# Kernel tuning notes

Measured on AMD Instinct MI355X. Metric: run time of the kernel, lower is better.

## Reference

```python
import jax, jax.numpy as jnp
import numpy as np

NMAX = 1
MARGIN = 0.2
N, D = 16384, 256

def setup_inputs() -> dict:
    key = jax.random.key(0)
    k1, k2 = jax.random.split(key)
    imgs = jax.random.normal(k1, (N, D), dtype=jnp.float32)
    caps = jax.random.normal(k2, (N, D), dtype=jnp.float32)
    return {"imgs": imgs, "caps": caps}

def reference(imgs, caps):
    # scores[i, j] = <img_i, cap_j>
    scores = imgs @ caps.T                      # [N, N]
    diag = jnp.diagonal(scores)                 # [N]
    s = scores - 2.0 * jnp.diag(diag)
    # hardest negatives per caption (top over image axis = rows) -> [nmax, N]
    max_c = jax.lax.top_k(s.T, NMAX)[0].T
    # hardest negatives per image (top over caption axis = cols) -> [N, nmax]
    max_i = jax.lax.top_k(s, NMAX)[0]
    neg_cap = jnp.sum(jnp.maximum(max_c + (MARGIN - diag)[None, :], 0.0))
    neg_img = jnp.sum(jnp.maximum(max_i + (MARGIN - diag)[:, None], 0.0))
    return neg_cap + neg_img
```

## Files before the change

### kernel.cpp

```cpp
#include <hip/hip_runtime.h>
#include <hip/hip_bf16.h>
#include <hip/hip_fp8.h>
#include <stdint.h>
#include <math.h>

#define NN 16384
#define DD 256
#define MARGIN_F 0.2f

typedef __attribute__((ext_vector_type(8))) int int32x8;
typedef __attribute__((ext_vector_type(4))) float f32x4;

__device__ inline unsigned fkey(float f) {
    unsigned b = __float_as_uint(f);
    return (b & 0x80000000u) ? ~b : (b | 0x80000000u);
}
__device__ inline float fdec(unsigned k) {
    return __uint_as_float((k & 0x80000000u) ? (k ^ 0x80000000u) : ~k);
}
#define NEG_INF_KEY 0x007FFFFFu

__device__ inline void gload16(const void* g, void* l) {
    __builtin_amdgcn_global_load_lds(
        (const __attribute__((address_space(1))) void*)g,
        (__attribute__((address_space(3))) void*)l, 16, 0, 0);
}

__device__ inline unsigned pk8(float4 v) {
    __hip_fp8_e4m3 q0(v.x), q1(v.y), q2(v.z), q3(v.w);
    return (unsigned)q0.__x | ((unsigned)q1.__x << 8) |
           ((unsigned)q2.__x << 16) | ((unsigned)q3.__x << 24);
}

__global__ __launch_bounds__(256) void fused_prep_kernel(
    const float* __restrict__ imgs, const float* __restrict__ caps,
    unsigned char* __restrict__ imgs8, unsigned char* __restrict__ caps8,
    float* __restrict__ diag, unsigned* __restrict__ rowmax,
    unsigned* __restrict__ colmax) {
    const int i = (blockIdx.x << 2) + (threadIdx.x >> 6);
    const int l = threadIdx.x & 63;
    const float4* a4 = reinterpret_cast<const float4*>(imgs + (size_t)i * DD);
    const float4* b4 = reinterpret_cast<const float4*>(caps + (size_t)i * DD);
    float4 av = a4[l];
    float4 bv = b4[l];
    reinterpret_cast<unsigned*>(imgs8 + (size_t)i * DD)[l] = pk8(av);
    reinterpret_cast<unsigned*>(caps8 + (size_t)i * DD)[l] = pk8(bv);
    float s = av.x * bv.x + av.y * bv.y + av.z * bv.z + av.w * bv.w;
    #pragma unroll
    for (int off = 32; off > 0; off >>= 1) s += __shfl_down(s, off);
    if (l == 0) {
        diag[i] = s;
        rowmax[i] = NEG_INF_KEY;
        colmax[i] = NEG_INF_KEY;
    }
}

__global__ __launch_bounds__(256, 2) void score_max_kernel(
    const unsigned char* __restrict__ imgs8,
    const unsigned char* __restrict__ caps8,
    const float* __restrict__ diag,
    unsigned* __restrict__ rowmax, unsigned* __restrict__ colmax) {

    __shared__ char lds[49152];
    unsigned* clds = reinterpret_cast<unsigned*>(lds + 32768);

    const int bid   = blockIdx.x;
    const int panel = bid >> 2;
    const int strip = bid & 3;
    const int brow  = panel << 7;
    const int scol  = strip << 12;

    const int t    = threadIdx.x;
    const int wid  = t >> 6;
    const int lane = t & 63;
    const int wr   = wid >> 1;
    const int wc   = wid & 1;
    const int rg   = lane >> 4;
    const int cl   = lane & 15;

    #pragma unroll
    for (int i = 0; i < 16; ++i) clds[t + (i << 8)] = NEG_INF_KEY;

    const int sl = t & 15;
    const int rw = t >> 4;
    const int srcoff = (((sl >> 1) ^ (rw & 7)) << 5) + ((sl & 1) << 4);

    {
        const unsigned char* src = imgs8 + (((size_t)(brow + rw)) << 8) + srcoff;
        #pragma unroll
        for (int i = 0; i < 8; ++i)
            gload16(src + ((size_t)i << 12), lds + t * 16 + i * 4096);
    }
    __syncthreads();

    int32x8 af[4][2];
    #pragma unroll
    for (int m = 0; m < 4; ++m) {
        const int row = wr * 64 + m * 16 + cl;
        #pragma unroll
        for (int ks = 0; ks < 2; ++ks)
            af[m][ks] = *reinterpret_cast<const int32x8*>(
                lds + row * 256 + (((rg + (ks << 2)) ^ (cl & 7)) << 5));
    }
    __syncthreads();

    #define STAGEB(bo, cb) {                                                   \
        const unsigned char* s_ =                                              \
            caps8 + (((size_t)((cb) + rw)) << 8) + srcoff;                     \
        _Pragma("unroll")                                                      \
        for (int i_ = 0; i_ < 4; ++i_)                                         \
            gload16(s_ + ((size_t)i_ << 12), lds + (bo) + t * 16 + i_ * 4096); \
    }

    STAGEB(0, scol);

    float rmx[4][4];
    #pragma unroll
    for (int m = 0; m < 4; ++m)
        #pragma unroll
        for (int r = 0; r < 4; ++r) rmx[m][r] = -INFINITY;

    const int rr0 = wc * 32 + cl;
    unsigned boff[2];
    #pragma unroll
    for (int ks = 0; ks < 2; ++ks)
        boff[ks] = rr0 * 256 + (((rg + (ks << 2)) ^ (cl & 7)) << 5);

    const f32x4 zv = (f32x4){0.f, 0.f, 0.f, 0.f};
    #define SCL 0x7F7F7F7F

    for (int h = 0; h < 64; ++h) {
        const int cb = scol + (h << 6);
        const char* cur = lds + ((h & 1) << 14);

        __builtin_amdgcn_s_barrier();
        asm volatile("" ::: "memory");
        if (h < 63) {
            STAGEB(((h + 1) & 1) << 14, cb + 64);
            asm volatile("s_waitcnt vmcnt(4)" ::: "memory");
        } else {
            asm volatile("s_waitcnt vmcnt(0)" ::: "memory");
        }
        __builtin_amdgcn_s_barrier();
        asm volatile("" ::: "memory");

        int32x8 b00 = *reinterpret_cast<const int32x8*>(cur + boff[0]);
        int32x8 b01 = *reinterpret_cast<const int32x8*>(cur + boff[0] + 4096);
        int32x8 b10 = *reinterpret_cast<const int32x8*>(cur + boff[1]);
        int32x8 b11 = *reinterpret_cast<const int32x8*>(cur + boff[1] + 4096);

        f32x4 acc[4][2];
        __builtin_amdgcn_s_setprio(1);
        #pragma unroll
        for (int m = 0; m < 4; ++m) {
            acc[m][0] = __builtin_amdgcn_mfma_scale_f32_16x16x128_f8f6f4(
                af[m][0], b00, zv, 0, 0, 0, SCL, 0, SCL);
            acc[m][1] = __builtin_amdgcn_mfma_scale_f32_16x16x128_f8f6f4(
                af[m][0], b01, zv, 0, 0, 0, SCL, 0, SCL);
        }
        #pragma unroll
        for (int m = 0; m < 4; ++m) {
            acc[m][0] = __builtin_amdgcn_mfma_scale_f32_16x16x128_f8f6f4(
                af[m][1], b10, acc[m][0], 0, 0, 0, SCL, 0, SCL);
            acc[m][1] = __builtin_amdgcn_mfma_scale_f32_16x16x128_f8f6f4(
                af[m][1], b11, acc[m][1], 0, 0, 0, SCL, 0, SCL);
        }
        __builtin_amdgcn_s_setprio(0);

        if (cb < brow + 128 && cb + 64 > brow) {
            #pragma unroll
            for (int m = 0; m < 4; ++m)
                #pragma unroll
                for (int r = 0; r < 4; ++r) {
                    const int i = brow + wr * 64 + m * 16 + (rg << 2) + r;
                    const int d = i - cb - wc * 32;
                    #pragma unroll
                    for (int n = 0; n < 2; ++n)
                        if (d == n * 16 + cl) acc[m][n][r] = -diag[i];
                }
        }

        #pragma unroll
        for (int m = 0; m < 4; ++m)
            #pragma unroll
            for (int r = 0; r < 4; ++r)
                rmx[m][r] = fmaxf(rmx[m][r],
                                  fmaxf(acc[m][0][r], acc[m][1][r]));

        #pragma unroll
        for (int n = 0; n < 2; ++n) {
            float v = acc[0][n][0];
            #pragma unroll
            for (int m = 0; m < 4; ++m)
                #pragma unroll
                for (int r = 0; r < 4; ++r)
                    v = fmaxf(v, acc[m][n][r]);
            v = fmaxf(v, __shfl_xor(v, 16));
            v = fmaxf(v, __shfl_xor(v, 32));
            if (rg == 0)
                atomicMax(&clds[(h << 6) + wc * 32 + n * 16 + cl], fkey(v));
        }
    }

    __syncthreads();
    #pragma unroll
    for (int i = 0; i < 16; ++i) {
        const int c = t + (i << 8);
        atomicMax(&colmax[scol + c], clds[c]);
    }

    #pragma unroll
    for (int m = 0; m < 4; ++m)
        #pragma unroll
        for (int r = 0; r < 4; ++r) {
            float v = rmx[m][r];
            v = fmaxf(v, __shfl_xor(v, 1));
            v = fmaxf(v, __shfl_xor(v, 2));
            v = fmaxf(v, __shfl_xor(v, 4));
            v = fmaxf(v, __shfl_xor(v, 8));
            if (cl == 0)
                atomicMax(&rowmax[brow + wr * 64 + m * 16 + (rg << 2) + r],
                          fkey(v));
        }
    #undef STAGEB
}

__global__ __launch_bounds__(1024) void finalize_kernel(
    const float* __restrict__ diag,
    const unsigned* __restrict__ rowmax,
    const unsigned* __restrict__ colmax,
    float* __restrict__ out) {
    __shared__ float red[1024];
    int t = threadIdx.x;
    float s = 0.f;
    for (int idx = t; idx < 2 * NN; idx += 1024) {
        int i = idx & (NN - 1);
        float mx = fdec((idx < NN) ? colmax[i] : rowmax[i]);
        s += fmaxf(mx + (MARGIN_F - diag[i]), 0.f);
    }
    red[t] = s;
    __syncthreads();
    for (int off = 512; off > 0; off >>= 1) {
        if (t < off) red[t] += red[t + off];
        __syncthreads();
    }
    if (t == 0) out[0] = red[0];
}

extern "C" void kernel_launch(void* const* d_in, const int* in_sizes, int n_in,
                              void* d_out, int out_size, void* d_ws, size_t ws_size,
                              hipStream_t stream) {
    const float* imgs = reinterpret_cast<const float*>(d_in[0]);
    const float* caps = reinterpret_cast<const float*>(d_in[1]);

    float* diag          = reinterpret_cast<float*>(d_ws);
    unsigned* rowmax     = reinterpret_cast<unsigned*>(diag + NN);
    unsigned* colmax     = rowmax + NN;
    unsigned char* imgs8 = reinterpret_cast<unsigned char*>(colmax + NN);
    unsigned char* caps8 = imgs8 + (size_t)NN * DD;

    fused_prep_kernel<<<NN / 4, 256, 0, stream>>>(imgs, caps, imgs8, caps8,
                                                  diag, rowmax, colmax);

    score_max_kernel<<<512, 256, 0, stream>>>(imgs8, caps8, diag,
                                              rowmax, colmax);

    finalize_kernel<<<1, 1024, 0, stream>>>(diag, rowmax, colmax,
                                            reinterpret_cast<float*>(d_out));
}
```

Baseline: 110.0 us.

## Stage 128-column caption tiles per barrier and write column maxima directly to global

Each pipeline step now loads 128 caption rows into a 32KB double-buffered LDS tile and processes two 64-column sub-blocks, halving the number of barrier-synchronised iterations. The shared-memory column-max buffer and its final flush are removed; per-column maxima are atomically merged straight into global colmax. The max reductions are also rebalanced into pairwise trees. This cuts barrier and wait overhead per compute step but raises LDS to 64KB, which may limit occupancy, and adds many more global atomics.

```diff
diff --git a/kernel.cpp b/kernel.cpp
--- a/kernel.cpp
+++ b/kernel.cpp
@@ -61,8 +61,7 @@
     const float* __restrict__ diag,
     unsigned* __restrict__ rowmax, unsigned* __restrict__ colmax) {
 
-    __shared__ char lds[49152];
-    unsigned* clds = reinterpret_cast<unsigned*>(lds + 32768);
+    __shared__ char lds[65536];
 
     const int bid   = blockIdx.x;
     const int panel = bid >> 2;
@@ -71,16 +70,13 @@
     const int scol  = strip << 12;
 
     const int t    = threadIdx.x;
+    const int lane = t & 63;
     const int wid  = t >> 6;
-    const int lane = t & 63;
     const int wr   = wid >> 1;
     const int wc   = wid & 1;
     const int rg   = lane >> 4;
     const int cl   = lane & 15;
 
-    #pragma unroll
-    for (int i = 0; i < 16; ++i) clds[t + (i << 8)] = NEG_INF_KEY;
-
     const int sl = t & 15;
     const int rw = t >> 4;
     const int srcoff = (((sl >> 1) ^ (rw & 7)) << 5) + ((sl & 1) << 4);
@@ -108,7 +104,7 @@
         const unsigned char* s_ =                                              \
             caps8 + (((size_t)((cb) + rw)) << 8) + srcoff;                     \
         _Pragma("unroll")                                                      \
-        for (int i_ = 0; i_ < 4; ++i_)                                         \
+        for (int i_ = 0; i_ < 8; ++i_)                                         \
             gload16(s_ + ((size_t)i_ << 12), lds + (bo) + t * 16 + i_ * 4096); \
     }
 
@@ -129,84 +125,84 @@
     const f32x4 zv = (f32x4){0.f, 0.f, 0.f, 0.f};
     #define SCL 0x7F7F7F7F
 
-    for (int h = 0; h < 64; ++h) {
-        const int cb = scol + (h << 6);
-        const char* cur = lds + ((h & 1) << 14);
+    for (int h = 0; h < 32; ++h) {
+        const int cb = scol + (h << 7);
+        const char* cur = lds + ((h & 1) << 15);
 
         __builtin_amdgcn_s_barrier();
         asm volatile("" ::: "memory");
-        if (h < 63) {
-            STAGEB(((h + 1) & 1) << 14, cb + 64);
-            asm volatile("s_waitcnt vmcnt(4)" ::: "memory");
+        if (h < 31) {
+            STAGEB(((h + 1) & 1) << 15, cb + 128);
+            asm volatile("s_waitcnt vmcnt(8)" ::: "memory");
         } else {
             asm volatile("s_waitcnt vmcnt(0)" ::: "memory");
         }
         __builtin_amdgcn_s_barrier();
         asm volatile("" ::: "memory");
 
-        int32x8 b00 = *reinterpret_cast<const int32x8*>(cur + boff[0]);
-        int32x8 b01 = *reinterpret_cast<const int32x8*>(cur + boff[0] + 4096);
-        int32x8 b10 = *reinterpret_cast<const int32x8*>(cur + boff[1]);
-        int32x8 b11 = *reinterpret_cast<const int32x8*>(cur + boff[1] + 4096);
-
-        f32x4 acc[4][2];
-        __builtin_amdgcn_s_setprio(1);
-        #pragma unroll
-        for (int m = 0; m < 4; ++m) {
-            acc[m][0] = __builtin_amdgcn_mfma_scale_f32_16x16x128_f8f6f4(
-                af[m][0], b00, zv, 0, 0, 0, SCL, 0, SCL);
-            acc[m][1] = __builtin_amdgcn_mfma_scale_f32_16x16x128_f8f6f4(
-                af[m][0], b01, zv, 0, 0, 0, SCL, 0, SCL);
-        }
-        #pragma unroll
-        for (int m = 0; m < 4; ++m) {
-            acc[m][0] = __builtin_amdgcn_mfma_scale_f32_16x16x128_f8f6f4(
-                af[m][1], b10, acc[m][0], 0, 0, 0, SCL, 0, SCL);
-            acc[m][1] = __builtin_amdgcn_mfma_scale_f32_16x16x128_f8f6f4(
-                af[m][1], b11, acc[m][1], 0, 0, 0, SCL, 0, SCL);
-        }
-        __builtin_amdgcn_s_setprio(0);
-
-        if (cb < brow + 128 && cb + 64 > brow) {
-            #pragma unroll
-            for (int m = 0; m < 4; ++m)
+        #pragma unroll
+        for (int c = 0; c < 2; ++c) {
+            const int cbh = cb + (c << 6);
+            const char* sb = cur + (c << 14);
+
+            int32x8 b00 = *reinterpret_cast<const int32x8*>(sb + boff[0]);
+            int32x8 b01 = *reinterpret_cast<const int32x8*>(sb + boff[0] + 4096);
+            int32x8 b10 = *reinterpret_cast<const int32x8*>(sb + boff[1]);
+            int32x8 b11 = *reinterpret_cast<const int32x8*>(sb + boff[1] + 4096);
+
+            f32x4 acc[4][2];
+            __builtin_amdgcn_s_setprio(1);
+            #pragma unroll
+            for (int m = 0; m < 4; ++m) {
+                acc[m][0] = __builtin_amdgcn_mfma_scale_f32_16x16x128_f8f6f4(
+                    af[m][0], b00, zv, 0, 0, 0, SCL, 0, SCL);
+                acc[m][1] = __builtin_amdgcn_mfma_scale_f32_16x16x128_f8f6f4(
+                    af[m][0], b01, zv, 0, 0, 0, SCL, 0, SCL);
+            }
+            #pragma unroll
+            for (int m = 0; m < 4; ++m) {
+                acc[m][0] = __builtin_amdgcn_mfma_scale_f32_16x16x128_f8f6f4(
+                    af[m][1], b10, acc[m][0], 0, 0, 0, SCL, 0, SCL);
+                acc[m][1] = __builtin_amdgcn_mfma_scale_f32_16x16x128_f8f6f4(
+                    af[m][1], b11, acc[m][1], 0, 0, 0, SCL, 0, SCL);
+            }
+            __builtin_amdgcn_s_setprio(0);
+
+            if (cbh < brow + 128 && cbh + 64 > brow) {
                 #pragma unroll
-                for (int r = 0; r < 4; ++r) {
-                    const int i = brow + wr * 64 + m * 16 + (rg << 2) + r;
-                    const int d = i - cb - wc * 32;
+                for (int m = 0; m < 4; ++m)
                     #pragma unroll
-                    for (int n = 0; n < 2; ++n)
-                        if (d == n * 16 + cl) acc[m][n][r] = -diag[i];
-                }
-        }
-
-        #pragma unroll
-        for (int m = 0; m < 4; ++m)
-            #pragma unroll
-            for (int r = 0; r < 4; ++r)
-                rmx[m][r] = fmaxf(rmx[m][r],
-                                  fmaxf(acc[m][0][r], acc[m][1][r]));
-
-        #pragma unroll
-        for (int n = 0; n < 2; ++n) {
-            float v = acc[0][n][0];
+                    for (int r = 0; r < 4; ++r) {
+                        const int i = brow + wr * 64 + m * 16 + (rg << 2) + r;
+                        const int d = i - cbh - wc * 32;
+                        #pragma unroll
+                        for (int n = 0; n < 2; ++n)
+                            if (d == n * 16 + cl) acc[m][n][r] = -diag[i];
+                    }
+            }
+
             #pragma unroll
             for (int m = 0; m < 4; ++m)
                 #pragma unroll
                 for (int r = 0; r < 4; ++r)
-                    v = fmaxf(v, acc[m][n][r]);
-            v = fmaxf(v, __shfl_xor(v, 16));
-            v = fmaxf(v, __shfl_xor(v, 32));
-            if (rg == 0)
-                atomicMax(&clds[(h << 6) + wc * 32 + n * 16 + cl], fkey(v));
+                    rmx[m][r] = fmaxf(fmaxf(rmx[m][r], acc[m][0][r]),
+                                      acc[m][1][r]);
+
+            #pragma unroll
+            for (int n = 0; n < 2; ++n) {
+                float v = fmaxf(fmaxf(acc[0][n][0], acc[0][n][1]),
+                                fmaxf(acc[0][n][2], acc[0][n][3]));
+                #pragma unroll
+                for (int m = 1; m < 4; ++m) {
+                    v = fmaxf(fmaxf(v, acc[m][n][0]), acc[m][n][1]);
+                    v = fmaxf(fmaxf(v, acc[m][n][2]), acc[m][n][3]);
+                }
+                v = fmaxf(v, __shfl_xor(v, 16));
+                v = fmaxf(v, __shfl_xor(v, 32));
+                if (rg == 0)
+                    atomicMax(&colmax[cbh + wc * 32 + n * 16 + cl], fkey(v));
+            }
         }
-    }
-
-    __syncthreads();
-    #pragma unroll
-    for (int i = 0; i < 16; ++i) {
-        const int c = t + (i << 8);
-        atomicMax(&colmax[scol + c], clds[c]);
     }
 
     #pragma unroll
```

New measurement: 118.9 us. +8.1%, slower.
